# Optimization experiments

Hardware: AMD Instinct MI355X
Metric: run time of the kernel (lower is better)

The kernel has to match this reference:

```python
import jax, jax.numpy as jnp
import numpy as np

B_SZ, N_INST, N_FEAT, N_HID, C, M = 2048, 8, 100, 40, 40, 41


def setup_inputs() -> dict:
    key = jax.random.key(0)
    k_x, k_m, k_a, k_b = jax.random.split(key, 4)
    x = jax.random.normal(k_x, (B_SZ, N_INST, N_FEAT), dtype=jnp.float32)
    # binary top-k style gate over components (b, i, C)
    topk_mask = (jax.random.uniform(k_m, (B_SZ, N_INST, C)) < 0.25).astype(jnp.float32)
    A = jax.random.normal(k_a, (N_INST, C, N_FEAT, M), dtype=jnp.float32) * 0.02
    Bp = jax.random.normal(k_b, (N_INST, C, M, N_HID), dtype=jnp.float32) * 0.02
    b_final = jnp.zeros((N_INST, N_FEAT), dtype=jnp.float32)
    return {"x": x, "topk_mask": topk_mask, "A": A, "Bp": Bp, "b_final": b_final}


def reference(x, topk_mask, A, Bp, b_final):
    # linear1: low-rank component projection with gating
    # inner: (b, i, C, m)
    inner1 = jnp.einsum('bif,icfm->bicm', x, A)
    inner1 = inner1 * topk_mask[..., None]
    # contract m and sum over components C -> (b, i, n_hidden)
    h = jnp.einsum('bicm,icmh->bih', inner1, Bp)
    # linear2 (transposed): A2 = B^T (i,C,h,m), B2 = A^T (i,C,m,f)
    inner2 = jnp.einsum('bih,icmh->bicm', h, Bp)
    inner2 = inner2 * topk_mask[..., None]
    out = jnp.einsum('bicm,icfm->bif', inner2, A)
    return jax.nn.relu(out + b_final)
```

## Files before the change

### kernel.cpp

```cpp
#include <hip/hip_runtime.h>

#define NI 8
#define NF 100
#define NH 40
#define NC 40
#define NM 41
#define BSZ 2048
#define BT 64
#define XPAD 104
#define MSTR 68

typedef __attribute__((ext_vector_type(8))) short bf16x8;
typedef __attribute__((ext_vector_type(4))) float f32x4;
typedef __attribute__((ext_vector_type(4))) unsigned int u32x4;

__device__ __forceinline__ unsigned short f2bf(float f) {
    unsigned int u = __builtin_bit_cast(unsigned int, f);
    u += 0x7fffu + ((u >> 16) & 1u);
    return (unsigned short)(u >> 16);
}
__device__ __forceinline__ float bf2f(unsigned short s) {
    unsigned int u = ((unsigned int)s) << 16;
    return __builtin_bit_cast(float, u);
}
__device__ __forceinline__ bf16x8 pack8(float4 u, float4 v) {
    u32x4 w;
    w.x = (unsigned int)f2bf(u.x) | ((unsigned int)f2bf(u.y) << 16);
    w.y = (unsigned int)f2bf(u.z) | ((unsigned int)f2bf(u.w) << 16);
    w.z = (unsigned int)f2bf(v.x) | ((unsigned int)f2bf(v.y) << 16);
    w.w = (unsigned int)f2bf(v.z) | ((unsigned int)f2bf(v.w) << 16);
    return __builtin_bit_cast(bf16x8, w);
}

__global__ __launch_bounds__(512) void build_w_kernel(
    const float* __restrict__ A, const float* __restrict__ Bp,
    unsigned short* __restrict__ Wb1, unsigned short* __restrict__ Wb2)
{
    __shared__ __align__(16) float As[NF * NM];
    __shared__ __align__(16) float Bs[NM * NH];
    __shared__ __align__(16) float Ws[NF * NH];
    const int ic = blockIdx.x;
    const float* Ap  = A  + (size_t)ic * NF * NM;
    const float* Bpp = Bp + (size_t)ic * NM * NH;
    for (int idx = threadIdx.x; idx < NF * NM; idx += 512) As[idx] = Ap[idx];
    for (int idx = threadIdx.x; idx < NM * NH; idx += 512) Bs[idx] = Bpp[idx];
    __syncthreads();
    for (int idx = threadIdx.x; idx < NF * (NH / 4); idx += 512) {
        const int f  = idx / (NH / 4);
        const int hq = idx % (NH / 4);
        float4 acc = make_float4(0.f, 0.f, 0.f, 0.f);
        #pragma unroll
        for (int m = 0; m < NM; ++m) {
            const float  a = As[f * NM + m];
            const float4 b = *(const float4*)&Bs[m * NH + hq * 4];
            acc.x += a * b.x; acc.y += a * b.y; acc.z += a * b.z; acc.w += a * b.w;
        }
        *(float4*)&Ws[f * NH + hq * 4] = acc;
    }
    __syncthreads();

    for (int e = threadIdx.x; e < 768; e += 512) {
        const int nt = e >> 8, k = (e >> 6) & 3, ln = e & 63;
        const int colx = ln & 15, quad = ln >> 4;
        const int h = nt * 16 + colx;
        unsigned int w[4];
        #pragma unroll
        for (int jj = 0; jj < 4; ++jj) {
            const int f0 = k * 32 + quad * 8 + jj * 2;
            const int f1 = f0 + 1;
            const unsigned int lo = (f0 < NF && h < NH) ? f2bf(Ws[f0 * NH + h]) : 0;
            const unsigned int hi = (f1 < NF && h < NH) ? f2bf(Ws[f1 * NH + h]) : 0;
            w[jj] = lo | (hi << 16);
        }
        ((u32x4*)Wb1)[(size_t)ic * 768 + e] = (u32x4){w[0], w[1], w[2], w[3]};
    }
    for (int e = threadIdx.x; e < 896; e += 512) {
        const int nt = e >> 7, kk = (e >> 6) & 1, ln = e & 63;
        const int colx = ln & 15, quad = ln >> 4;
        const int f = nt * 16 + colx;
        unsigned int w[4];
        #pragma unroll
        for (int jj = 0; jj < 4; ++jj) {
            const int h0 = kk * 32 + quad * 8 + jj * 2;
            const int h1 = h0 + 1;
            const unsigned int lo = (f < NF && h0 < NH) ? f2bf(Ws[f * NH + h0]) : 0;
            const unsigned int hi = (f < NF && h1 < NH) ? f2bf(Ws[f * NH + h1]) : 0;
            w[jj] = lo | (hi << 16);
        }
        ((u32x4*)Wb2)[(size_t)ic * 896 + e] = (u32x4){w[0], w[1], w[2], w[3]};
    }
}

__global__ __launch_bounds__(512, 1) void fused_kernel(
    const float* __restrict__ x, const float* __restrict__ mask,
    const float* __restrict__ b_final,
    const unsigned short* __restrict__ Wb1, const unsigned short* __restrict__ Wb2,
    float* __restrict__ out)
{
    __shared__ __align__(16) float msxT[NC * MSTR];
    __shared__ __align__(16) unsigned char regionB[57344];
    unsigned short* region = (unsigned short*)regionB;
    float* xs = (float*)regionB;

    const int tid  = threadIdx.x;
    const int lane = tid & 63;
    const int wav  = tid >> 6;
    const int col  = lane & 15;
    const int quad = lane >> 4;
    const int i    = blockIdx.x % NI;
    const int b0   = (blockIdx.x / NI) * BT;

    const u32x4* wb1i = (const u32x4*)Wb1 + (size_t)i * NC * 768;
    const u32x4* wb2i = (const u32x4*)Wb2 + (size_t)i * NC * 896;

    u32x4 bufA[12];
    {
        const u32x4* p = wb1i + (size_t)wav * 768;
        #pragma unroll
        for (int e = 0; e < 12; ++e) bufA[e] = p[e * 64 + lane];
    }

    for (int idx = tid; idx < BT * NC; idx += 512) {
        const int b = idx / NC, c = idx % NC;
        msxT[c * MSTR + b] = mask[((size_t)(b0 + b) * NI + i) * NC + c];
    }
    for (int idx = tid; idx < BT * (XPAD / 4); idx += 512) {
        const int row = idx / (XPAD / 4), fq = idx % (XPAD / 4);
        float4 v = make_float4(0.f, 0.f, 0.f, 0.f);
        if (fq < NF / 4)
            v = *(const float4*)(x + ((size_t)(b0 + row) * NI + i) * NF + fq * 4);
        *(float4*)&xs[row * XPAD + fq * 4] = v;
    }
    __syncthreads();

    bf16x8 a1[4][4];
    #pragma unroll
    for (int mt = 0; mt < 4; ++mt) {
        const float* xr = xs + (mt * 16 + col) * XPAD;
        #pragma unroll
        for (int k = 0; k < 4; ++k) {
            if (k < 3 || quad == 0)
                a1[mt][k] = pack8(*(const float4*)(xr + k * 32 + quad * 8),
                                  *(const float4*)(xr + k * 32 + quad * 8 + 4));
            else
                a1[mt][k] = __builtin_bit_cast(bf16x8, (u32x4){0, 0, 0, 0});
        }
    }
    __syncthreads();

    f32x4 H[4][3];
    #pragma unroll
    for (int mt = 0; mt < 4; ++mt)
        #pragma unroll
        for (int nt = 0; nt < 3; ++nt)
            H[mt][nt] = (f32x4){0.f, 0.f, 0.f, 0.f};

    #pragma unroll 1
    for (int cc = 0; cc < NC / 8; ++cc) {
        const int c = wav + cc * 8;
        #pragma unroll
        for (int nt = 0; nt < 3; ++nt) {
            #pragma unroll
            for (int mt = 0; mt < 4; ++mt) {
                f32x4 P = (f32x4){0.f, 0.f, 0.f, 0.f};
                #pragma unroll
                for (int k = 0; k < 4; ++k)
                    P = __builtin_amdgcn_mfma_f32_16x16x32_bf16(
                        a1[mt][k], __builtin_bit_cast(bf16x8, bufA[nt * 4 + k]), P, 0, 0, 0);
                const float4 mv = *(const float4*)&msxT[c * MSTR + mt * 16 + quad * 4];
                H[mt][nt][0] += mv.x * P[0];
                H[mt][nt][1] += mv.y * P[1];
                H[mt][nt][2] += mv.z * P[2];
                H[mt][nt][3] += mv.w * P[3];
            }
            if (cc < NC / 8 - 1) {
                const u32x4* p = wb1i + (size_t)(c + 8) * 768;
                #pragma unroll
                for (int k = 0; k < 4; ++k)
                    bufA[nt * 4 + k] = p[(nt * 4 + k) * 64 + lane];
            }
        }
    }

    const int fh  = wav >> 2;
    const int cp  = wav & 3;
    const int ne  = fh ? 3 : 4;
    const int nb  = fh * 4;

    u32x4 buf2A[8];
    {
        const u32x4* p = wb2i + (size_t)cp * 896;
        #pragma unroll
        for (int j = 0; j < 4; ++j) {
            #pragma unroll
            for (int kk = 0; kk < 2; ++kk) {
                buf2A[j * 2 + kk] = (u32x4){0, 0, 0, 0};
                if (j < ne)
                    buf2A[j * 2 + kk] = p[((nb + j) * 2 + kk) * 64 + lane];
            }
        }
    }

    #pragma unroll
    for (int mt = 0; mt < 4; ++mt)
        #pragma unroll
        for (int nt = 0; nt < 3; ++nt)
            #pragma unroll
            for (int r = 0; r < 4; ++r) {
                const int b = mt * 16 + quad * 4 + r;
                const int h = nt * 16 + col;
                region[(wav * 64 + b) * 48 + h] = f2bf(H[mt][nt][r]);
            }
    __syncthreads();

    for (int idx = tid; idx < BT * 48; idx += 512) {
        const int b = idx / 48, h = idx % 48;
        float s = 0.f;
        #pragma unroll
        for (int g = 0; g < 8; ++g) s += bf2f(region[(g * 64 + b) * 48 + h]);
        region[b * 48 + h] = (h < NH) ? f2bf(s) : (unsigned short)0;
    }
    __syncthreads();

    bf16x8 a2[4][2];
    #pragma unroll
    for (int mt = 0; mt < 4; ++mt) {
        const int b = mt * 16 + col;
        #pragma unroll
        for (int kk = 0; kk < 2; ++kk)
            a2[mt][kk] = *(const bf16x8*)&region[b * 48 + kk * 32 + quad * 8];
    }
    __syncthreads();

    f32x4 Ot[4][4];
    #pragma unroll
    for (int mt = 0; mt < 4; ++mt)
        #pragma unroll
        for (int j = 0; j < 4; ++j)
            Ot[mt][j] = (f32x4){0.f, 0.f, 0.f, 0.f};

    #pragma unroll 1
    for (int cc = 0; cc < NC / 4; ++cc) {
        const int c = cp + cc * 4;
        #pragma unroll
        for (int j = 0; j < 4; ++j) {
            if (j < ne) {
                #pragma unroll
                for (int mt = 0; mt < 4; ++mt) {
                    f32x4 P = (f32x4){0.f, 0.f, 0.f, 0.f};
                    P = __builtin_amdgcn_mfma_f32_16x16x32_bf16(
                        a2[mt][0], __builtin_bit_cast(bf16x8, buf2A[j * 2 + 0]), P, 0, 0, 0);
                    P = __builtin_amdgcn_mfma_f32_16x16x32_bf16(
                        a2[mt][1], __builtin_bit_cast(bf16x8, buf2A[j * 2 + 1]), P, 0, 0, 0);
                    const float4 mv = *(const float4*)&msxT[c * MSTR + mt * 16 + quad * 4];
                    Ot[mt][j][0] += mv.x * P[0];
                    Ot[mt][j][1] += mv.y * P[1];
                    Ot[mt][j][2] += mv.z * P[2];
                    Ot[mt][j][3] += mv.w * P[3];
                }
                if (cc < NC / 4 - 1) {
                    const u32x4* p = wb2i + (size_t)(c + 4) * 896;
                    #pragma unroll
                    for (int kk = 0; kk < 2; ++kk)
                        buf2A[j * 2 + kk] = p[((nb + j) * 2 + kk) * 64 + lane];
                }
            }
        }
    }

    #pragma unroll
    for (int mt = 0; mt < 4; ++mt)
        #pragma unroll
        for (int j = 0; j < 4; ++j) {
            if (j < ne) {
                const int f = (nb + j) * 16 + col;
                if (f < NF) {
                    #pragma unroll
                    for (int r = 0; r < 4; ++r) {
                        const int b = mt * 16 + quad * 4 + r;
                        region[(cp * 64 + b) * 112 + f] = f2bf(Ot[mt][j][r]);
                    }
                }
            }
        }
    __syncthreads();

    for (int idx = tid; idx < BT * NF; idx += 512) {
        const int b = idx / NF, f = idx % NF;
        float s = 0.f;
        #pragma unroll
        for (int p = 0; p < 4; ++p)
            s += bf2f(region[(p * 64 + b) * 112 + f]);
        const float v = s + b_final[i * NF + f];
        out[((size_t)(b0 + b) * NI + i) * NF + f] = fmaxf(v, 0.f);
    }
}

extern "C" void kernel_launch(void* const* d_in, const int* in_sizes, int n_in,
                              void* d_out, int out_size, void* d_ws, size_t ws_size,
                              hipStream_t stream) {
    const float* x       = (const float*)d_in[0];
    const float* tk_mask = (const float*)d_in[1];
    const float* A       = (const float*)d_in[2];
    const float* Bp      = (const float*)d_in[3];
    const float* b_final = (const float*)d_in[4];
    float* out = (float*)d_out;

    unsigned short* Wb1 = (unsigned short*)d_ws;
    unsigned short* Wb2 = Wb1 + (size_t)NI * NC * 768 * 8;

    build_w_kernel<<<NI * NC, 512, 0, stream>>>(A, Bp, Wb1, Wb2);
    fused_kernel<<<(BSZ / BT) * NI, 512, 0, stream>>>(x, tk_mask, b_final, Wb1, Wb2, out);
}
```

Baseline: 105.4 us.

## Merge weight-build and fused kernels into one cooperative launch with grid sync

Folds the per-(instance,component) weight-precompute kernel into the main fused kernel. Each of the 256 blocks builds one or two W tiles into workspace while also staging its x and mask tiles, then a grid-wide cooperative sync makes the weights visible before the MFMA phase. This removes a separate kernel launch and its gap and overlaps weight building with input staging. The cost is a grid barrier, uneven work because 64 blocks build two tiles, and a larger shared-memory footprint.

```diff
diff --git a/kernel.cpp b/kernel.cpp
--- a/kernel.cpp
+++ b/kernel.cpp
@@ -1,4 +1,5 @@
 #include <hip/hip_runtime.h>
+#include <hip/hip_cooperative_groups.h>
 
 #define NI 8
 #define NF 100
@@ -32,75 +33,20 @@
     return __builtin_bit_cast(bf16x8, w);
 }
 
-__global__ __launch_bounds__(512) void build_w_kernel(
+__global__ __launch_bounds__(512, 1) void merged_kernel(
+    const float* __restrict__ x, const float* __restrict__ mask,
     const float* __restrict__ A, const float* __restrict__ Bp,
-    unsigned short* __restrict__ Wb1, unsigned short* __restrict__ Wb2)
-{
-    __shared__ __align__(16) float As[NF * NM];
-    __shared__ __align__(16) float Bs[NM * NH];
-    __shared__ __align__(16) float Ws[NF * NH];
-    const int ic = blockIdx.x;
-    const float* Ap  = A  + (size_t)ic * NF * NM;
-    const float* Bpp = Bp + (size_t)ic * NM * NH;
-    for (int idx = threadIdx.x; idx < NF * NM; idx += 512) As[idx] = Ap[idx];
-    for (int idx = threadIdx.x; idx < NM * NH; idx += 512) Bs[idx] = Bpp[idx];
-    __syncthreads();
-    for (int idx = threadIdx.x; idx < NF * (NH / 4); idx += 512) {
-        const int f  = idx / (NH / 4);
-        const int hq = idx % (NH / 4);
-        float4 acc = make_float4(0.f, 0.f, 0.f, 0.f);
-        #pragma unroll
-        for (int m = 0; m < NM; ++m) {
-            const float  a = As[f * NM + m];
-            const float4 b = *(const float4*)&Bs[m * NH + hq * 4];
-            acc.x += a * b.x; acc.y += a * b.y; acc.z += a * b.z; acc.w += a * b.w;
-        }
-        *(float4*)&Ws[f * NH + hq * 4] = acc;
-    }
-    __syncthreads();
-
-    for (int e = threadIdx.x; e < 768; e += 512) {
-        const int nt = e >> 8, k = (e >> 6) & 3, ln = e & 63;
-        const int colx = ln & 15, quad = ln >> 4;
-        const int h = nt * 16 + colx;
-        unsigned int w[4];
-        #pragma unroll
-        for (int jj = 0; jj < 4; ++jj) {
-            const int f0 = k * 32 + quad * 8 + jj * 2;
-            const int f1 = f0 + 1;
-            const unsigned int lo = (f0 < NF && h < NH) ? f2bf(Ws[f0 * NH + h]) : 0;
-            const unsigned int hi = (f1 < NF && h < NH) ? f2bf(Ws[f1 * NH + h]) : 0;
-            w[jj] = lo | (hi << 16);
-        }
-        ((u32x4*)Wb1)[(size_t)ic * 768 + e] = (u32x4){w[0], w[1], w[2], w[3]};
-    }
-    for (int e = threadIdx.x; e < 896; e += 512) {
-        const int nt = e >> 7, kk = (e >> 6) & 1, ln = e & 63;
-        const int colx = ln & 15, quad = ln >> 4;
-        const int f = nt * 16 + colx;
-        unsigned int w[4];
-        #pragma unroll
-        for (int jj = 0; jj < 4; ++jj) {
-            const int h0 = kk * 32 + quad * 8 + jj * 2;
-            const int h1 = h0 + 1;
-            const unsigned int lo = (f < NF && h0 < NH) ? f2bf(Ws[f * NH + h0]) : 0;
-            const unsigned int hi = (f < NF && h1 < NH) ? f2bf(Ws[f * NH + h1]) : 0;
-            w[jj] = lo | (hi << 16);
-        }
-        ((u32x4*)Wb2)[(size_t)ic * 896 + e] = (u32x4){w[0], w[1], w[2], w[3]};
-    }
-}
-
-__global__ __launch_bounds__(512, 1) void fused_kernel(
-    const float* __restrict__ x, const float* __restrict__ mask,
     const float* __restrict__ b_final,
-    const unsigned short* __restrict__ Wb1, const unsigned short* __restrict__ Wb2,
+    unsigned short* __restrict__ Wb1, unsigned short* __restrict__ Wb2,
     float* __restrict__ out)
 {
     __shared__ __align__(16) float msxT[NC * MSTR];
-    __shared__ __align__(16) unsigned char regionB[57344];
+    __shared__ __align__(16) unsigned char regionB[71680];
     unsigned short* region = (unsigned short*)regionB;
     float* xs = (float*)regionB;
+    float* As = (float*)(regionB + 26624);
+    float* Bs = (float*)(regionB + 43024);
+    float* Ws = (float*)(regionB + 49584);
 
     const int tid  = threadIdx.x;
     const int lane = tid & 63;
@@ -110,16 +56,6 @@
     const int i    = blockIdx.x % NI;
     const int b0   = (blockIdx.x / NI) * BT;
 
-    const u32x4* wb1i = (const u32x4*)Wb1 + (size_t)i * NC * 768;
-    const u32x4* wb2i = (const u32x4*)Wb2 + (size_t)i * NC * 896;
-
-    u32x4 bufA[12];
-    {
-        const u32x4* p = wb1i + (size_t)wav * 768;
-        #pragma unroll
-        for (int e = 0; e < 12; ++e) bufA[e] = p[e * 64 + lane];
-    }
-
     for (int idx = tid; idx < BT * NC; idx += 512) {
         const int b = idx / NC, c = idx % NC;
         msxT[c * MSTR + b] = mask[((size_t)(b0 + b) * NI + i) * NC + c];
@@ -131,7 +67,60 @@
             v = *(const float4*)(x + ((size_t)(b0 + row) * NI + i) * NF + fq * 4);
         *(float4*)&xs[row * XPAD + fq * 4] = v;
     }
-    __syncthreads();
+
+    const int nu = (blockIdx.x < 64) ? 2 : 1;
+    for (int t = 0; t < nu; ++t) {
+        const int ic = blockIdx.x + t * 256;
+        const float* Ap  = A  + (size_t)ic * NF * NM;
+        const float* Bpp = Bp + (size_t)ic * NM * NH;
+        for (int idx = tid; idx < NF * NM; idx += 512) As[idx] = Ap[idx];
+        for (int idx = tid; idx < NM * NH; idx += 512) Bs[idx] = Bpp[idx];
+        __syncthreads();
+        for (int idx = tid; idx < NF * (NH / 4); idx += 512) {
+            const int f  = idx / (NH / 4);
+            const int hq = idx % (NH / 4);
+            float4 acc = make_float4(0.f, 0.f, 0.f, 0.f);
+            #pragma unroll
+            for (int m = 0; m < NM; ++m) {
+                const float  a = As[f * NM + m];
+                const float4 b = *(const float4*)&Bs[m * NH + hq * 4];
+                acc.x += a * b.x; acc.y += a * b.y; acc.z += a * b.z; acc.w += a * b.w;
+            }
+            *(float4*)&Ws[f * NH + hq * 4] = acc;
+        }
+        __syncthreads();
+        for (int e = tid; e < 768; e += 512) {
+            const int nt = e >> 8, k = (e >> 6) & 3, ln = e & 63;
+            const int colx = ln & 15, qd = ln >> 4;
+            const int h = nt * 16 + colx;
+            unsigned int w[4];
+            #pragma unroll
+            for (int jj = 0; jj < 4; ++jj) {
+                const int f0 = k * 32 + qd * 8 + jj * 2;
+                const int f1 = f0 + 1;
+                const unsigned int lo = (f0 < NF && h < NH) ? f2bf(Ws[f0 * NH + h]) : 0;
+                const unsigned int hi = (f1 < NF && h < NH) ? f2bf(Ws[f1 * NH + h]) : 0;
+                w[jj] = lo | (hi << 16);
+            }
+            ((u32x4*)Wb1)[(size_t)ic * 768 + e] = (u32x4){w[0], w[1], w[2], w[3]};
+        }
+        for (int e = tid; e < 896; e += 512) {
+            const int nt = e >> 7, kk = (e >> 6) & 1, ln = e & 63;
+            const int colx = ln & 15, qd = ln >> 4;
+            const int f = nt * 16 + colx;
+            unsigned int w[4];
+            #pragma unroll
+            for (int jj = 0; jj < 4; ++jj) {
+                const int h0 = kk * 32 + qd * 8 + jj * 2;
+                const int h1 = h0 + 1;
+                const unsigned int lo = (f < NF && h0 < NH) ? f2bf(Ws[f * NH + h0]) : 0;
+                const unsigned int hi = (f < NF && h1 < NH) ? f2bf(Ws[f * NH + h1]) : 0;
+                w[jj] = lo | (hi << 16);
+            }
+            ((u32x4*)Wb2)[(size_t)ic * 896 + e] = (u32x4){w[0], w[1], w[2], w[3]};
+        }
+        __syncthreads();
+    }
 
     bf16x8 a1[4][4];
     #pragma unroll
@@ -146,7 +135,19 @@
                 a1[mt][k] = __builtin_bit_cast(bf16x8, (u32x4){0, 0, 0, 0});
         }
     }
-    __syncthreads();
+
+    __threadfence();
+    cooperative_groups::this_grid().sync();
+
+    const u32x4* wb1i = (const u32x4*)Wb1 + (size_t)i * NC * 768;
+    const u32x4* wb2i = (const u32x4*)Wb2 + (size_t)i * NC * 896;
+
+    u32x4 bufA[12];
+    {
+        const u32x4* p = wb1i + (size_t)wav * 768;
+        #pragma unroll
+        for (int e = 0; e < 12; ++e) bufA[e] = p[e * 64 + lane];
+    }
 
     f32x4 H[4][3];
     #pragma unroll
@@ -309,6 +310,8 @@
     unsigned short* Wb1 = (unsigned short*)d_ws;
     unsigned short* Wb2 = Wb1 + (size_t)NI * NC * 768 * 8;
 
-    build_w_kernel<<<NI * NC, 512, 0, stream>>>(A, Bp, Wb1, Wb2);
-    fused_kernel<<<(BSZ / BT) * NI, 512, 0, stream>>>(x, tk_mask, b_final, Wb1, Wb2, out);
-}
+    void* args[] = {(void*)&x, (void*)&tk_mask, (void*)&A, (void*)&Bp,
+                    (void*)&b_final, (void*)&Wb1, (void*)&Wb2, (void*)&out};
+    hipLaunchCooperativeKernel((void*)merged_kernel, dim3((BSZ / BT) * NI),
+                               dim3(512), args, 0, stream);
+}
```

New measurement: 191.3 us. +81.4%, slower.
